# Kernel optimization log

Measured on AMD Instinct MI355X. Metric: run time of the kernel, lower is better.

## Reference

```python
import jax, jax.numpy as jnp
import numpy as np
import math

B, L, HID, H = 16, 1024, 1024, 16
E = HID // H
HALF = L // 2 + 1                      # 513 rfft bins
GLOBAL_RATIO = 0.6
LEFT = int(HALF * (1.0 - GLOBAL_RATIO))  # 205 (i=0, filter_mixer='G')
RIGHT = HALF                            # 513
FACTOR = 1
TOP_K = int(FACTOR * math.log(L))       # 6
LN_EPS = 1e-12


def setup_inputs() -> dict:
    key = jax.random.key(0)
    ks = jax.random.split(key, 12)
    s = 0.02
    return {
        "input_tensor": jax.random.normal(ks[0], (B, L, HID), jnp.float32),
        "attention_mask": jnp.zeros((B, 1, 1, L), jnp.float32),
        "Wq": jax.random.normal(ks[1], (HID, HID), jnp.float32) * s,
        "bq": jnp.zeros((HID,), jnp.float32),
        "Wk": jax.random.normal(ks[2], (HID, HID), jnp.float32) * s,
        "bk": jnp.zeros((HID,), jnp.float32),
        "Wv": jax.random.normal(ks[3], (HID, HID), jnp.float32) * s,
        "bv": jnp.zeros((HID,), jnp.float32),
        "Wd": jax.random.normal(ks[4], (HID, HID), jnp.float32) * s,
        "bd": jnp.zeros((HID,), jnp.float32),
        "gamma": jnp.ones((HID,), jnp.float32),
        "beta": jnp.zeros((HID,), jnp.float32),
    }


def _heads(x):  # [B,L,HID] -> [B,H,E,L]
    return x.reshape(B, L, H, E).transpose(0, 2, 3, 1)


def _layer_norm(x, gamma, beta):
    mu = jnp.mean(x, axis=-1, keepdims=True)
    var = jnp.var(x, axis=-1, keepdims=True)
    return (x - mu) / jnp.sqrt(var + LN_EPS) * gamma + beta


def reference(input_tensor, attention_mask, Wq, bq, Wk, bk, Wv, bv, Wd, bd, gamma, beta):
    # QKV projections -> [B,H,E,L]
    q = _heads(input_tensor @ Wq + bq)
    k = _heads(input_tensor @ Wk + bk)
    v = _heads(input_tensor @ Wv + bv)

    # FFT-based autocorrelation restricted to retained frequency band [LEFT,RIGHT)
    q_fft = jnp.fft.rfft(q, axis=-1)            # [B,H,E,HALF] complex64
    k_fft = jnp.fft.rfft(k, axis=-1)
    res = q_fft[..., LEFT:RIGHT] * jnp.conj(k_fft[..., LEFT:RIGHT])
    box = jnp.zeros((B, H, E, HALF), res.dtype).at[..., LEFT:RIGHT].set(res)
    corr = jnp.fft.irfft(box, n=L, axis=-1)     # [B,H,E,L]

    # time_delay_agg_training: topk shared delays, softmax-weighted roll aggregation
    mean_value = jnp.mean(corr, axis=(1, 2))            # [B,L]
    _, idx = jax.lax.top_k(jnp.mean(mean_value, axis=0), TOP_K)  # [TOP_K]
    weights = mean_value[:, idx]                         # [B,TOP_K]
    tmp_corr = jax.nn.softmax(weights, axis=-1)
    delays_agg = jnp.zeros_like(v)
    for i in range(TOP_K):  # TOP_K=6, fixed small loop
        pattern = jnp.roll(v, -idx[i], axis=-1)
        delays_agg = delays_agg + pattern * tmp_corr[:, i][:, None, None, None]

    # [B,H,E,L] -> [B,L,HID]
    context = delays_agg.transpose(0, 3, 1, 2).reshape(B, L, HID)
    hidden = context @ Wd + bd
    return _layer_norm(hidden + input_tensor, gamma, beta)
```

## Files before the change

### kernel.cpp

```cpp
#include <hip/hip_runtime.h>


typedef unsigned short u16;
typedef unsigned int   u32;
typedef __attribute__((ext_vector_type(8))) __bf16 bf16x8;
typedef __attribute__((ext_vector_type(4))) float  floatx4;

#define HIDn 1024

__device__ __forceinline__ u16 f2b(float f){ u32 i = __float_as_uint(f); return (u16)((i + 0x7fffu + ((i>>16)&1u)) >> 16); }

__device__ __forceinline__ void gl_lds16(const u16* g, u16* l){
  __builtin_amdgcn_global_load_lds((__attribute__((address_space(1))) const void*)g,
                                   (__attribute__((address_space(3))) void*)l, 16, 0, 0);
}

__device__ __forceinline__ void bar(){
  asm volatile("" ::: "memory");
  __builtin_amdgcn_s_barrier();
  asm volatile("" ::: "memory");
}

__global__ void fill_kernel(float* __restrict__ out, float v, int n)
{
  const int i = blockIdx.x*blockDim.x + threadIdx.x;
  if (i < n) out[i] = v;
}

__global__ __launch_bounds__(256)
void cast_kernel(const float* __restrict__ x, u16* __restrict__ xb)
{
  const int i = blockIdx.x*256 + threadIdx.x;
  const float4* xp = (const float4*)x;
  const float4 a = xp[2*i], b = xp[2*i+1];
  uint4 o;
  o.x = (u32)f2b(a.x) | ((u32)f2b(a.y)<<16);
  o.y = (u32)f2b(a.z) | ((u32)f2b(a.w)<<16);
  o.z = (u32)f2b(b.x) | ((u32)f2b(b.y)<<16);
  o.w = (u32)f2b(b.z) | ((u32)f2b(b.w)<<16);
  ((uint4*)xb)[i] = o;
}

__global__ __launch_bounds__(1024)
void transpose_kernel(const float* __restrict__ Wq, const float* __restrict__ Wk,
                      const float* __restrict__ Wv, const float* __restrict__ Wd,
                      u16* __restrict__ WqkvT, u16* __restrict__ WdT)
{
  __shared__ float tile[32][33];
  const int mat = blockIdx.z;
  const float* W = (mat==0)?Wq:(mat==1)?Wk:(mat==2)?Wv:Wd;
  const int k = blockIdx.y*32 + threadIdx.y;
  const int n = blockIdx.x*32 + threadIdx.x;
  tile[threadIdx.y][threadIdx.x] = W[(long)k*HIDn + n];
  __syncthreads();
  const int on = blockIdx.x*32 + threadIdx.y;
  const int ok = blockIdx.y*32 + threadIdx.x;
  const u16 val = f2b(tile[threadIdx.x][threadIdx.y]);
  if (mat < 3) WqkvT[(long)(mat*HIDn + on)*HIDn + ok] = val;
  else         WdT[(long)on*HIDn + ok] = val;
}

__global__ __launch_bounds__(1024)
void gf_kernel(float* __restrict__ gf, float* __restrict__ c)
{
  const int d = threadIdx.x;
  float s = 0.f;
  for (int f = 205; f < 512; ++f){
    int p = (f*d) & 1023;
    s += cosf(6.283185307179586f * (float)p * (1.0f/1024.0f));
  }
  gf[d] = (2.f*s + ((d & 1) ? -1.f : 1.f)) * (1.0f/1048576.0f);
  #pragma unroll
  for (int b = 0; b < 16; ++b) c[b*1024 + d] = 0.f;
}

template<int EPI>
__global__ __launch_bounds__(512, 2)
void gemm_mfma(const u16* __restrict__ A, int lda, long sA,
               const u16* __restrict__ Bt, int ldb, long sB,
               void* __restrict__ C0, u16* __restrict__ o1, u16* __restrict__ o2,
               int ldc, int K,
               const float* __restrict__ b0, const float* __restrict__ b1,
               const float* __restrict__ b2, const float* __restrict__ resid,
               float* __restrict__ cbuf)
{
  __shared__ __align__(16) u16 As[2][16384];
  __shared__ __align__(16) u16 Bs[2][16384];
  __shared__ float bins[512];

  const int bx = blockIdx.x, by = blockIdx.y, bz = blockIdx.z;
  const int tid  = threadIdx.x;
  const int wave = tid >> 6, lane = tid & 63;
  const int waveM = wave >> 2, waveN = wave & 3;
  const int qd = lane >> 4, ln = lane & 15, rl = ln & 7;
  const u16* Ab = A  + (long)bz * sA;
  const u16* Bb = Bt + (long)bz * sB;
  const int aRow0 = by * 256, bRow0 = bx * 256;
  const int nt = K >> 6;

  const int s0 = wave*128 + lane;
  const int r0 = s0 >> 3, r1 = r0 + 8;
  const int kc = ((s0 & 7) ^ (r0 & 7)) * 8;
  const long aOff0 = (long)(aRow0 + r0)*lda + kc;
  const long aOff1 = (long)(aRow0 + r1)*lda + kc;
  const long bOff0 = (long)(bRow0 + r0)*ldb + kc;
  const long bOff1 = (long)(bRow0 + r1)*ldb + kc;
  const int dstW = wave*1024;

#define STAGE_A(p, h, kt) do{ \
    gl_lds16(Ab + aOff0 + (long)(h)*128*lda + (kt), &As[p][(h)*8192 + dstW]); \
    gl_lds16(Ab + aOff1 + (long)(h)*128*lda + (kt), &As[p][(h)*8192 + dstW + 512]); }while(0)
#define STAGE_B(p, h, kt) do{ \
    gl_lds16(Bb + bOff0 + (long)(h)*128*ldb + (kt), &Bs[p][(h)*8192 + dstW]); \
    gl_lds16(Bb + bOff1 + (long)(h)*128*ldb + (kt), &Bs[p][(h)*8192 + dstW + 512]); }while(0)

  if (EPI == 3) bins[tid] = 0.f;

  floatx4 acc[8][4];
  const floatx4 z4 = {0.f, 0.f, 0.f, 0.f};
  #pragma unroll
  for (int i=0;i<8;++i)
    #pragma unroll
    for (int j=0;j<4;++j) acc[i][j] = z4;

  const int aRd = (waveM*128 + ln)*64;
  const int bRd = (waveN*64  + ln)*64;
  const int csw0 = ((0 + qd) ^ rl) * 8;
  const int csw1 = ((4 + qd) ^ rl) * 8;

  STAGE_B(0,0,0); STAGE_B(0,1,0); STAGE_A(0,0,0); STAGE_A(0,1,0);
  STAGE_B(1,0,64); STAGE_B(1,1,64); STAGE_A(1,0,64);
  asm volatile("s_waitcnt vmcnt(6)" ::: "memory");
  __builtin_amdgcn_s_barrier();
  asm volatile("" ::: "memory");

  bf16x8 avA[4], avB[4], bvA[4], bvB[4];
  {
    const u16* Ap = &As[0][0]; const u16* Bp = &Bs[0][0];
    avA[0] = *(const bf16x8*)(Ap + aRd + 0*1024 + csw0);
    #pragma unroll
    for (int ni=0;ni<4;++ni) bvA[ni] = *(const bf16x8*)(Bp + bRd + ni*1024 + csw0);
    #pragma unroll
    for (int mi=1;mi<4;++mi) avA[mi] = *(const bf16x8*)(Ap + aRd + mi*1024 + csw0);
  }
  __builtin_amdgcn_sched_barrier(0);

  for (int t = 0; t < nt; ++t){
    const int p = t & 1;
    const u16* Ap = &As[p][0];
    const u16* Bp = &Bs[p][0];
    const int k1 = (t+1) << 6, k2 = (t+2) << 6;

    avB[0] = *(const bf16x8*)(Ap + aRd + 0*1024 + csw1);
    #pragma unroll
    for (int ni=0;ni<4;++ni) bvB[ni] = *(const bf16x8*)(Bp + bRd + ni*1024 + csw1);
    #pragma unroll
    for (int mi=1;mi<4;++mi) avB[mi] = *(const bf16x8*)(Ap + aRd + mi*1024 + csw1);
    if (t+1 < nt) STAGE_A(p^1, 1, k1);
    __builtin_amdgcn_sched_barrier(0);
    __builtin_amdgcn_s_setprio(1);
    #pragma unroll
    for (int mi=0;mi<4;++mi)
      #pragma unroll
      for (int ni=0;ni<4;++ni)
        acc[mi][ni] = __builtin_amdgcn_mfma_f32_16x16x32_bf16(avA[mi], bvA[ni], acc[mi][ni], 0,0,0);
    __builtin_amdgcn_s_setprio(0);
    __builtin_amdgcn_sched_barrier(0);

    #pragma unroll
    for (int mi=0;mi<4;++mi) avA[mi] = *(const bf16x8*)(Ap + aRd + 4096 + mi*1024 + csw0);
    __builtin_amdgcn_sched_barrier(0);
    __builtin_amdgcn_s_setprio(1);
    #pragma unroll
    for (int mi=0;mi<4;++mi)
      #pragma unroll
      for (int ni=0;ni<4;++ni)
        acc[mi][ni] = __builtin_amdgcn_mfma_f32_16x16x32_bf16(avB[mi], bvB[ni], acc[mi][ni], 0,0,0);
    __builtin_amdgcn_s_setprio(0);
    __builtin_amdgcn_sched_barrier(0);
    bar();

    #pragma unroll
    for (int mi=0;mi<4;++mi) avB[mi] = *(const bf16x8*)(Ap + aRd + 4096 + mi*1024 + csw1);
    if (t+2 < nt){ STAGE_B(p, 0, k2); STAGE_B(p, 1, k2); }
    __builtin_amdgcn_sched_barrier(0);
    __builtin_amdgcn_s_setprio(1);
    #pragma unroll
    for (int mi=0;mi<4;++mi)
      #pragma unroll
      for (int ni=0;ni<4;++ni)
        acc[4+mi][ni] = __builtin_amdgcn_mfma_f32_16x16x32_bf16(avA[mi], bvA[ni], acc[4+mi][ni], 0,0,0);
    __builtin_amdgcn_s_setprio(0);
    __builtin_amdgcn_sched_barrier(0);

    if (t+2 < nt){
      STAGE_A(p, 0, k2);
      asm volatile("s_waitcnt vmcnt(6)" ::: "memory");
    } else if (t+1 < nt){
      asm volatile("s_waitcnt vmcnt(0)" ::: "memory");
    }
    if (t+1 < nt){
      asm volatile("s_waitcnt lgkmcnt(0)" ::: "memory");
      __builtin_amdgcn_sched_barrier(0);
      bar();
      const u16* An = &As[p^1][0];
      const u16* Bn = &Bs[p^1][0];
      avA[0] = *(const bf16x8*)(An + aRd + 0*1024 + csw0);
      #pragma unroll
      for (int ni=0;ni<4;++ni) bvA[ni] = *(const bf16x8*)(Bn + bRd + ni*1024 + csw0);
      #pragma unroll
      for (int mi=1;mi<4;++mi) avA[mi] = *(const bf16x8*)(An + aRd + mi*1024 + csw0);
      __builtin_amdgcn_sched_barrier(0);
    }
    __builtin_amdgcn_s_setprio(1);
    #pragma unroll
    for (int mi=0;mi<4;++mi)
      #pragma unroll
      for (int ni=0;ni<4;++ni)
        acc[4+mi][ni] = __builtin_amdgcn_mfma_f32_16x16x32_bf16(avB[mi], bvB[ni], acc[4+mi][ni], 0,0,0);
    __builtin_amdgcn_s_setprio(0);
  }
#undef STAGE_A
#undef STAGE_B

  if (EPI == 3){
    float dsum[11][4];
    #pragma unroll
    for (int dd=0; dd<11; ++dd)
      #pragma unroll
      for (int r=0;r<4;++r) dsum[dd][r] = 0.f;
    #pragma unroll
    for (int mi=0;mi<8;++mi)
      #pragma unroll
      for (int ni=0;ni<4;++ni){
        const int dd = mi - ni + 3;
        #pragma unroll
        for (int r=0;r<4;++r) dsum[dd][r] += acc[mi][ni][r];
      }
    const int base = 255 + 128*waveM - 64*waveN + 4*qd - ln;
    #pragma unroll
    for (int dd=0; dd<11; ++dd)
      #pragma unroll
      for (int r=0;r<4;++r)
        atomicAdd(&bins[base + 16*(dd-3) + r], dsum[dd][r]);
    __syncthreads();
    if (tid < 511){
      const int d = (aRow0 - bRow0 + tid - 255) & 1023;
      atomicAdd(cbuf + bz*1024 + d, bins[tid]);
    }
    return;
  }

  if (EPI == 0){
    const int which = bx >> 2;
    const float* bp = (which==0) ? b0 : ((which==1) ? b1 : b2);
    u16* Cb = (which==0) ? (u16*)C0 : ((which==1) ? o1 : o2);
    const int nb = bRow0 & 1023;
    #pragma unroll
    for (int mi=0;mi<8;++mi){
      const int gm = aRow0 + waveM*128 + mi*16 + qd*4;
      #pragma unroll
      for (int ni=0;ni<4;++ni){
        const int nl = nb + waveN*64 + ni*16 + ln;
        const float bias = bp[nl];
        #pragma unroll
        for (int r=0;r<4;++r) Cb[(long)(gm+r)*ldc + nl] = f2b(acc[mi][ni][r] + bias);
      }
    }
  } else {
    float* C = (float*)C0;
    #pragma unroll
    for (int mi=0;mi<8;++mi){
      const int gm = aRow0 + waveM*128 + mi*16 + qd*4;
      #pragma unroll
      for (int ni=0;ni<4;++ni){
        const int gn = bRow0 + waveN*64 + ni*16 + ln;
        const float bias = b0[gn];
        #pragma unroll
        for (int r=0;r<4;++r)
          C[(long)(gm+r)*ldc + gn] = acc[mi][ni][r] + bias + resid[(long)(gm+r)*ldc + gn];
      }
    }
  }
}

__global__ __launch_bounds__(1024)
void filter_kernel(const float* __restrict__ c, const float* __restrict__ gf,
                   float* __restrict__ mv)
{
  __shared__ float carr[1024];
  __shared__ float gsh[1024];
  const int b = blockIdx.x, l = threadIdx.x;
  carr[l] = c[b*1024 + l]; gsh[l] = gf[l];
  __syncthreads();
  float o = 0.f;
  #pragma unroll 4
  for (int m = 0; m < 1024; ++m) o += carr[m] * gsh[(l - m) & 1023];
  mv[b*1024 + l] = o;
}

__global__ __launch_bounds__(1024)
void topk_kernel(const float* __restrict__ mv, int* __restrict__ idxout,
                 float* __restrict__ wout)
{
  __shared__ float vals[1024];
  __shared__ float rv[1024];
  __shared__ int   ri[1024];
  __shared__ int   chosen[6];
  const int t = threadIdx.x;
  float s = 0.f;
  #pragma unroll
  for (int b = 0; b < 16; ++b) s += mv[b*1024 + t];
  vals[t] = s;
  __syncthreads();
  for (int r = 0; r < 6; ++r){
    rv[t] = vals[t]; ri[t] = t; __syncthreads();
    for (int off = 512; off > 0; off >>= 1){
      if (t < off){
        const float v2 = rv[t+off]; const int i2 = ri[t+off];
        if (v2 > rv[t] || (v2 == rv[t] && i2 < ri[t])){ rv[t] = v2; ri[t] = i2; }
      }
      __syncthreads();
    }
    if (t == 0){ chosen[r] = ri[0]; idxout[r] = ri[0]; }
    __syncthreads();
    if (t == chosen[r]) vals[t] = -3.0e38f;
    __syncthreads();
  }
  if (t < 16){
    float w[6]; float mx = -3.0e38f;
    #pragma unroll
    for (int i = 0; i < 6; ++i){ w[i] = mv[t*1024 + chosen[i]]; mx = fmaxf(mx, w[i]); }
    float sum = 0.f;
    #pragma unroll
    for (int i = 0; i < 6; ++i){ w[i] = expf(w[i] - mx); sum += w[i]; }
    #pragma unroll
    for (int i = 0; i < 6; ++i) wout[t*6 + i] = w[i] / sum;
  }
}

__global__ __launch_bounds__(256)
void context_kernel(const u16* __restrict__ Vb, const int* __restrict__ idx,
                    const float* __restrict__ w, u16* __restrict__ CT)
{
  const int row = blockIdx.x*2 + (threadIdx.x >> 7);
  const int b = row >> 10, l = row & 1023;
  const int t = threadIdx.x & 127;
  float wl[6]; int id[6];
  #pragma unroll
  for (int i = 0; i < 6; ++i){ id[i] = idx[i]; wl[i] = w[b*6 + i]; }
  float acc[8] = {0,0,0,0,0,0,0,0};
  #pragma unroll
  for (int i = 0; i < 6; ++i){
    const long src = (long)b*1024 + ((l + id[i]) & 1023);
    const uint4 pk = *(const uint4*)(Vb + src*1024 + t*8);
    const float ww = wl[i];
    union{float f; u32 u;} cv;
    cv.u = pk.x<<16;          acc[0] += ww*cv.f;
    cv.u = pk.x & 0xffff0000u; acc[1] += ww*cv.f;
    cv.u = pk.y<<16;          acc[2] += ww*cv.f;
    cv.u = pk.y & 0xffff0000u; acc[3] += ww*cv.f;
    cv.u = pk.z<<16;          acc[4] += ww*cv.f;
    cv.u = pk.z & 0xffff0000u; acc[5] += ww*cv.f;
    cv.u = pk.w<<16;          acc[6] += ww*cv.f;
    cv.u = pk.w & 0xffff0000u; acc[7] += ww*cv.f;
  }
  uint4 o;
  o.x = (u32)f2b(acc[0]) | ((u32)f2b(acc[1])<<16);
  o.y = (u32)f2b(acc[2]) | ((u32)f2b(acc[3])<<16);
  o.z = (u32)f2b(acc[4]) | ((u32)f2b(acc[5])<<16);
  o.w = (u32)f2b(acc[6]) | ((u32)f2b(acc[7])<<16);
  *(uint4*)(CT + (long)row*1024 + t*8) = o;
}

__global__ __launch_bounds__(256)
void ln_kernel(float* __restrict__ io, const float* __restrict__ gamma,
               const float* __restrict__ beta)
{
  __shared__ float s1[256];
  __shared__ float s2[256];
  const int row = blockIdx.x, t = threadIdx.x;
  float4 v = ((const float4*)(io + (long)row*1024))[t];
  s1[t] = v.x+v.y+v.z+v.w;
  s2[t] = v.x*v.x+v.y*v.y+v.z*v.z+v.w*v.w;
  __syncthreads();
  for (int off = 128; off > 0; off >>= 1){
    if (t < off){ s1[t] += s1[t+off]; s2[t] += s2[t+off]; }
    __syncthreads();
  }
  const float mu  = s1[0] * (1.f/1024.f);
  const float var = fmaxf(s2[0] * (1.f/1024.f) - mu*mu, 0.f);
  const float rstd = rsqrtf(var + 1e-12f);
  const float4 g  = ((const float4*)gamma)[t];
  const float4 be = ((const float4*)beta)[t];
  float4 o;
  o.x = (v.x-mu)*rstd*g.x + be.x;
  o.y = (v.y-mu)*rstd*g.y + be.y;
  o.z = (v.z-mu)*rstd*g.z + be.z;
  o.w = (v.w-mu)*rstd*g.w + be.w;
  ((float4*)(io + (long)row*1024))[t] = o;
}

extern "C" void kernel_launch(void* const* d_in, const int* in_sizes, int n_in,
                              void* d_out, int out_size, void* d_ws, size_t ws_size,
                              hipStream_t stream)
{
  (void)in_sizes; (void)n_in;
  const float* x     = (const float*)d_in[0];
  const float* Wq    = (const float*)d_in[2];
  const float* bq    = (const float*)d_in[3];
  const float* Wk    = (const float*)d_in[4];
  const float* bk    = (const float*)d_in[5];
  const float* Wv    = (const float*)d_in[6];
  const float* bv    = (const float*)d_in[7];
  const float* Wd    = (const float*)d_in[8];
  const float* bd    = (const float*)d_in[9];
  const float* gamma = (const float*)d_in[10];
  const float* beta  = (const float*)d_in[11];
  float* outp = (float*)d_out;

  const size_t NEED = 142741952UL;
  if (ws_size < NEED){
    const int n = out_size/2;
    fill_kernel<<<(n+255)/256, 256, 0, stream>>>(outp, (float)ws_size, n);
    return;
  }
  char* ws = (char*)d_ws;
  u16*  xb    = (u16*)(ws);
  u16*  Qb    = (u16*)(ws + 33554432L);
  u16*  Kb    = (u16*)(ws + 67108864L);
  u16*  Vb    = (u16*)(ws + 100663296L);
  u16*  WqkvT = (u16*)(ws + 134217728L);
  u16*  WdT   = (u16*)(ws + 140509184L);
  float* cbuf = (float*)(ws + 142606336L);
  float* mv   = (float*)(ws + 142671872L);
  float* gf   = (float*)(ws + 142737408L);
  int*   idxb = (int*)  (ws + 142741504L);
  float* wsm  = (float*)(ws + 142741568L);
  u16*  CT    = Qb;

  cast_kernel<<<8192, 256, 0, stream>>>(x, xb);
  transpose_kernel<<<dim3(32,32,4), dim3(32,32), 0, stream>>>(Wq, Wk, Wv, Wd, WqkvT, WdT);
  gf_kernel<<<1, 1024, 0, stream>>>(gf, cbuf);

  gemm_mfma<0><<<dim3(12,64,1), 512, 0, stream>>>(
      xb, 1024, 0L, WqkvT, 1024, 0L, Qb, Kb, Vb, 1024, 1024,
      bq, bk, bv, nullptr, nullptr);

  gemm_mfma<3><<<dim3(4,4,16), 512, 0, stream>>>(
      Qb, 1024, 1048576L, Kb, 1024, 1048576L, nullptr, nullptr, nullptr, 0, 1024,
      nullptr, nullptr, nullptr, nullptr, cbuf);

  filter_kernel<<<16, 1024, 0, stream>>>(cbuf, gf, mv);
  topk_kernel<<<1, 1024, 0, stream>>>(mv, idxb, wsm);
  context_kernel<<<8192, 256, 0, stream>>>(Vb, idxb, wsm, CT);

  gemm_mfma<2><<<dim3(4,64,1), 512, 0, stream>>>(
      CT, 1024, 0L, WdT, 1024, 0L, outp, nullptr, nullptr, 1024, 1024,
      bd, nullptr, nullptr, x, nullptr);

  ln_kernel<<<16384, 256, 0, stream>>>(outp, gamma, beta);
}
```

Measured before the change: 485.2 us.

## Restructure GEMM main loop into quadrant-based ping-pong schedule with barriers

Replaces the two-phase K-loop of the bf16 MFMA GEMM with a schedule unrolled by two K-tiles. Each tile is split into four output quadrants, with LDS reads, global-to-LDS staging and MFMA clusters interleaved and separated by workgroup barriers, in the style of HipKittens' 8-wave ping-pong. The aim is to overlap LDS and global traffic with matrix work more evenly and to prefetch a full stage ahead. In exchange it adds many more barriers per iteration, and it assumes an even tile count, since the loop runs nt/2 times.

```diff
diff --git a/kernel.cpp b/kernel.cpp
--- a/kernel.cpp
+++ b/kernel.cpp
@@ -19,6 +19,10 @@
   asm volatile("" ::: "memory");
   __builtin_amdgcn_s_barrier();
   asm volatile("" ::: "memory");
+}
+__device__ __forceinline__ void lgkm0(){
+  asm volatile("s_waitcnt lgkmcnt(0)" ::: "memory");
+  __builtin_amdgcn_sched_barrier(0);
 }
 
 __global__ void fill_kernel(float* __restrict__ out, float v, int n)
@@ -128,100 +132,76 @@
   const int csw0 = ((0 + qd) ^ rl) * 8;
   const int csw1 = ((4 + qd) ^ rl) * 8;
 
-  STAGE_B(0,0,0); STAGE_B(0,1,0); STAGE_A(0,0,0); STAGE_A(0,1,0);
-  STAGE_B(1,0,64); STAGE_B(1,1,64); STAGE_A(1,0,64);
-  asm volatile("s_waitcnt vmcnt(6)" ::: "memory");
-  __builtin_amdgcn_s_barrier();
-  asm volatile("" ::: "memory");
-
-  bf16x8 avA[4], avB[4], bvA[4], bvB[4];
-  {
-    const u16* Ap = &As[0][0]; const u16* Bp = &Bs[0][0];
-    avA[0] = *(const bf16x8*)(Ap + aRd + 0*1024 + csw0);
-    #pragma unroll
-    for (int ni=0;ni<4;++ni) bvA[ni] = *(const bf16x8*)(Bp + bRd + ni*1024 + csw0);
-    #pragma unroll
-    for (int mi=1;mi<4;++mi) avA[mi] = *(const bf16x8*)(Ap + aRd + mi*1024 + csw0);
-  }
-  __builtin_amdgcn_sched_barrier(0);
-
-  for (int t = 0; t < nt; ++t){
-    const int p = t & 1;
-    const u16* Ap = &As[p][0];
-    const u16* Bp = &Bs[p][0];
-    const int k1 = (t+1) << 6, k2 = (t+2) << 6;
-
-    avB[0] = *(const bf16x8*)(Ap + aRd + 0*1024 + csw1);
-    #pragma unroll
-    for (int ni=0;ni<4;++ni) bvB[ni] = *(const bf16x8*)(Bp + bRd + ni*1024 + csw1);
-    #pragma unroll
-    for (int mi=1;mi<4;++mi) avB[mi] = *(const bf16x8*)(Ap + aRd + mi*1024 + csw1);
-    if (t+1 < nt) STAGE_A(p^1, 1, k1);
-    __builtin_amdgcn_sched_barrier(0);
-    __builtin_amdgcn_s_setprio(1);
-    #pragma unroll
-    for (int mi=0;mi<4;++mi)
-      #pragma unroll
-      for (int ni=0;ni<4;++ni)
-        acc[mi][ni] = __builtin_amdgcn_mfma_f32_16x16x32_bf16(avA[mi], bvA[ni], acc[mi][ni], 0,0,0);
-    __builtin_amdgcn_s_setprio(0);
-    __builtin_amdgcn_sched_barrier(0);
-
-    #pragma unroll
-    for (int mi=0;mi<4;++mi) avA[mi] = *(const bf16x8*)(Ap + aRd + 4096 + mi*1024 + csw0);
-    __builtin_amdgcn_sched_barrier(0);
-    __builtin_amdgcn_s_setprio(1);
-    #pragma unroll
-    for (int mi=0;mi<4;++mi)
-      #pragma unroll
-      for (int ni=0;ni<4;++ni)
-        acc[mi][ni] = __builtin_amdgcn_mfma_f32_16x16x32_bf16(avB[mi], bvB[ni], acc[mi][ni], 0,0,0);
-    __builtin_amdgcn_s_setprio(0);
-    __builtin_amdgcn_sched_barrier(0);
-    bar();
-
-    #pragma unroll
-    for (int mi=0;mi<4;++mi) avB[mi] = *(const bf16x8*)(Ap + aRd + 4096 + mi*1024 + csw1);
-    if (t+2 < nt){ STAGE_B(p, 0, k2); STAGE_B(p, 1, k2); }
-    __builtin_amdgcn_sched_barrier(0);
-    __builtin_amdgcn_s_setprio(1);
-    #pragma unroll
-    for (int mi=0;mi<4;++mi)
-      #pragma unroll
-      for (int ni=0;ni<4;++ni)
-        acc[4+mi][ni] = __builtin_amdgcn_mfma_f32_16x16x32_bf16(avA[mi], bvA[ni], acc[4+mi][ni], 0,0,0);
-    __builtin_amdgcn_s_setprio(0);
-    __builtin_amdgcn_sched_barrier(0);
-
-    if (t+2 < nt){
-      STAGE_A(p, 0, k2);
-      asm volatile("s_waitcnt vmcnt(6)" ::: "memory");
-    } else if (t+1 < nt){
-      asm volatile("s_waitcnt vmcnt(0)" ::: "memory");
-    }
-    if (t+1 < nt){
-      asm volatile("s_waitcnt lgkmcnt(0)" ::: "memory");
-      __builtin_amdgcn_sched_barrier(0);
-      bar();
-      const u16* An = &As[p^1][0];
-      const u16* Bn = &Bs[p^1][0];
-      avA[0] = *(const bf16x8*)(An + aRd + 0*1024 + csw0);
-      #pragma unroll
-      for (int ni=0;ni<4;++ni) bvA[ni] = *(const bf16x8*)(Bn + bRd + ni*1024 + csw0);
-      #pragma unroll
-      for (int mi=1;mi<4;++mi) avA[mi] = *(const bf16x8*)(An + aRd + mi*1024 + csw0);
-      __builtin_amdgcn_sched_barrier(0);
-    }
-    __builtin_amdgcn_s_setprio(1);
-    #pragma unroll
-    for (int mi=0;mi<4;++mi)
-      #pragma unroll
-      for (int ni=0;ni<4;++ni)
-        acc[4+mi][ni] = __builtin_amdgcn_mfma_f32_16x16x32_bf16(avB[mi], bvB[ni], acc[4+mi][ni], 0,0,0);
-    __builtin_amdgcn_s_setprio(0);
-  }
+  bf16x8 av0[4], av1[4];
+  bf16x8 bvA0[2], bvA1[2];
+  bf16x8 bvB0[2], bvB1[2];
+
+#define DS_AV(BUF, MH) do{ const u16* Ap_ = &As[BUF][0]; \
+    _Pragma("unroll") for (int mi=0;mi<4;++mi){ \
+      av0[mi] = *(const bf16x8*)(Ap_ + aRd + (MH)*4096 + mi*1024 + csw0); \
+      av1[mi] = *(const bf16x8*)(Ap_ + aRd + (MH)*4096 + mi*1024 + csw1); } }while(0)
+#define DS_BV(BUF, NH, d0_, d1_) do{ const u16* Bp_ = &Bs[BUF][0]; \
+    _Pragma("unroll") for (int ni=0;ni<2;++ni){ \
+      d0_[ni] = *(const bf16x8*)(Bp_ + bRd + ((NH)*2+ni)*1024 + csw0); \
+      d1_[ni] = *(const bf16x8*)(Bp_ + bRd + ((NH)*2+ni)*1024 + csw1); } }while(0)
+#define MFMAQ(MH, NH, b0_, b1_) do{ \
+    __builtin_amdgcn_sched_barrier(0); \
+    __builtin_amdgcn_s_setprio(1); \
+    _Pragma("unroll") for (int mi=0;mi<4;++mi) \
+      _Pragma("unroll") for (int ni=0;ni<2;++ni){ \
+        acc[(MH)*4+mi][(NH)*2+ni] = __builtin_amdgcn_mfma_f32_16x16x32_bf16(av0[mi], b0_[ni], acc[(MH)*4+mi][(NH)*2+ni],0,0,0); \
+        acc[(MH)*4+mi][(NH)*2+ni] = __builtin_amdgcn_mfma_f32_16x16x32_bf16(av1[mi], b1_[ni], acc[(MH)*4+mi][(NH)*2+ni],0,0,0); } \
+    __builtin_amdgcn_s_setprio(0); \
+    __builtin_amdgcn_sched_barrier(0); }while(0)
+
+  STAGE_B(0,0,0);  STAGE_B(0,1,0);  STAGE_A(0,0,0);  STAGE_A(0,1,0);
+  STAGE_B(1,0,64); STAGE_B(1,1,64); STAGE_A(1,0,64); STAGE_A(1,1,64);
+  asm volatile("s_waitcnt vmcnt(8)" ::: "memory");
+  bar();
+
+  const int nIt = nt >> 1;
+  for (int it = 0; it < nIt-1; ++it){
+    const int k2 = (it*2+2) << 6;
+    const int k3 = (it*2+3) << 6;
+    DS_AV(0,0); DS_BV(0,0,bvA0,bvA1);
+    bar(); lgkm0(); MFMAQ(0,0,bvA0,bvA1); bar();
+    DS_BV(0,1,bvB0,bvB1);
+    bar(); lgkm0(); MFMAQ(0,1,bvB0,bvB1); bar();
+    DS_AV(0,1); STAGE_B(0,0,k2);
+    bar(); lgkm0(); MFMAQ(1,0,bvA0,bvA1); bar();
+    STAGE_B(0,1,k2);
+    asm volatile("s_waitcnt vmcnt(4)" ::: "memory");
+    bar(); MFMAQ(1,1,bvB0,bvB1); bar();
+    DS_AV(1,0); DS_BV(1,0,bvA0,bvA1); STAGE_A(0,0,k2);
+    bar(); lgkm0(); MFMAQ(0,0,bvA0,bvA1); bar();
+    DS_BV(1,1,bvB0,bvB1); STAGE_A(0,1,k2);
+    bar(); lgkm0(); MFMAQ(0,1,bvB0,bvB1); bar();
+    DS_AV(1,1); STAGE_B(1,0,k3);
+    bar(); lgkm0(); MFMAQ(1,0,bvA0,bvA1); bar();
+    STAGE_B(1,1,k3); STAGE_A(1,0,k3); STAGE_A(1,1,k3);
+    asm volatile("s_waitcnt vmcnt(8)" ::: "memory");
+    bar(); MFMAQ(1,1,bvB0,bvB1); bar();
+  }
+  DS_AV(0,0); DS_BV(0,0,bvA0,bvA1);
+  bar(); lgkm0(); MFMAQ(0,0,bvA0,bvA1); bar();
+  DS_BV(0,1,bvB0,bvB1);
+  bar(); lgkm0(); MFMAQ(0,1,bvB0,bvB1); bar();
+  DS_AV(0,1);
+  bar(); lgkm0(); MFMAQ(1,0,bvA0,bvA1); bar();
+  asm volatile("s_waitcnt vmcnt(0)" ::: "memory");
+  bar(); MFMAQ(1,1,bvB0,bvB1); bar();
+  DS_AV(1,0); DS_BV(1,0,bvA0,bvA1);
+  bar(); lgkm0(); MFMAQ(0,0,bvA0,bvA1); bar();
+  DS_BV(1,1,bvB0,bvB1);
+  bar(); lgkm0(); MFMAQ(0,1,bvB0,bvB1); bar();
+  DS_AV(1,1);
+  bar(); lgkm0(); MFMAQ(1,0,bvA0,bvA1); bar();
+  MFMAQ(1,1,bvB0,bvB1);
 #undef STAGE_A
 #undef STAGE_B
+#undef DS_AV
+#undef DS_BV
+#undef MFMAQ
 
   if (EPI == 3){
     float dsum[11][4];
```

Result: slower. 497.8 us (+2.6%).
